# Kernel optimization log

Measured on AMD Instinct MI355X. Metric: run time of the kernel, lower is better.

Reference implementation:

```python
import jax, jax.numpy as jnp
import numpy as np

B, T, N, F, C, H, O = 4, 8, 4096, 32, 32, 64, 1
RADIUS = 50.0   # adjacency_threshold on pairwise distance
EPS = 1e-5      # batchnorm eps


def setup_inputs() -> dict:
    key = jax.random.key(0)
    ks = jax.random.split(key, 8)
    x = jax.random.normal(ks[0], (B, T, N, F), jnp.float32)
    # dist_mat from random 2D node locations in a 1000x1000 area; avg degree ~32
    loc = jax.random.uniform(ks[1], (N, 2), jnp.float32) * 1000.0
    d2 = jnp.sum((loc[:, None, :] - loc[None, :, :]) ** 2, axis=-1)  # [N,N]
    adj = (d2 < RADIUS ** 2).astype(jnp.float32)                     # includes self (d=0)
    dinv = 1.0 / jnp.sqrt(jnp.maximum(adj.sum(-1), 1.0))
    adj_norm = adj * dinv[:, None] * dinv[None, :]                   # D^-1/2 A D^-1/2
    s = 0.05
    return dict(
        x=x,
        adj_norm=adj_norm,
        bn_gamma=jnp.ones((F,), jnp.float32),
        bn_beta=jnp.zeros((F,), jnp.float32),
        W_gcn=jax.random.normal(ks[2], (F, C), jnp.float32) * s,
        b_gcn=jnp.zeros((C,), jnp.float32),
        W_ih=jax.random.normal(ks[3], (C, 3 * H), jnp.float32) * s,
        W_hh=jax.random.normal(ks[4], (H, 3 * H), jnp.float32) * s,
        b_ih=jnp.zeros((3 * H,), jnp.float32),
        b_hh=jnp.zeros((3 * H,), jnp.float32),
        W_dense=jax.random.normal(ks[5], (H, O), jnp.float32) * s,
        b_dense=jnp.zeros((O,), jnp.float32),
    )


def reference(x, adj_norm, bn_gamma, bn_beta, W_gcn, b_gcn, W_ih, W_hh, b_ih, b_hh, W_dense, b_dense):
    # BatchNorm2d over feature channel (training-mode batch stats, biased var)
    mean = x.mean(axis=(0, 1, 2))
    var = x.var(axis=(0, 1, 2))
    xn = (x - mean) * jax.lax.rsqrt(var + EPS) * bn_gamma + bn_beta  # [B,T,N,F]
    # GCN association (same math every timestep -> batch over T)
    ya = jnp.einsum('mn,btnf->btmf', adj_norm, xn)                   # neighbor aggregate
    y = jnp.einsum('btnf,fc->btnc', ya, W_gcn) + b_gcn               # [B,T,N,C]
    # precompute input-gate projections, then scan GRU cell over time
    gi = jnp.einsum('btnc,ch->btnh', y, W_ih) + b_ih                 # [B,T,N,3H]
    gi = jnp.transpose(gi, (1, 0, 2, 3))                             # [T,B,N,3H]

    def step(h, g):
        gh = h @ W_hh + b_hh
        r = jax.nn.sigmoid(g[..., :H] + gh[..., :H])
        z = jax.nn.sigmoid(g[..., H:2 * H] + gh[..., H:2 * H])
        n = jnp.tanh(g[..., 2 * H:] + r * gh[..., 2 * H:])
        h_new = (1.0 - z) * n + z * h
        return h_new, h_new

    h0 = jnp.zeros((B, N, H), x.dtype)
    _, hs = jax.lax.scan(step, h0, gi)                               # [T,B,N,H]
    out = jnp.transpose(hs, (1, 0, 2, 3)) @ W_dense + b_dense        # [B,T,N,O]
    return out
```

## Files before the change

kernel.cpp:

```cpp
#include <hip/hip_runtime.h>
#include <hip/hip_bf16.h>
#include <stdint.h>

#define B_ 4
#define T_ 8
#define N_ 4096
#define F_ 32
#define BT_ (B_*T_)
#define ROWS_ (B_*N_)
#define CAP_ 128
#define EPS_ 1e-5f
#define NELEM_ (B_*T_*N_*F_)

#define WS_BNP    0
#define WS_ROWSUM 16384
#define WS_DEG    (WS_ROWSUM + 4096)
#define WS_FRG    (WS_DEG + 4096)
#define WS_PAIR   (WS_FRG + 52*256)
#define WS_XA     (WS_PAIR + 4096*CAP_*2)
#define WS_X16    (WS_XA + NELEM_)

typedef float v4f __attribute__((ext_vector_type(4)));
typedef _Float16 half8 __attribute__((ext_vector_type(8)));
union HU { uint32_t u[4]; half8 v; };

__device__ inline float sigm_f(float x) {
  return __builtin_amdgcn_rcpf(1.0f + __expf(-x));
}
__device__ inline uint32_t f16pair(float a, float b) {
  union { _Float16 h; unsigned short s; } x, y;
  x.h = (_Float16)a; y.h = (_Float16)b;
  return (uint32_t)x.s | ((uint32_t)y.s << 16);
}
__device__ inline void sp2(float a0, float a1, uint32_t& hi, uint32_t& lo) {
  _Float16 h0 = (_Float16)a0, h1 = (_Float16)a1;
  float r0 = a0 - (float)h0, r1 = a1 - (float)h1;
  union { _Float16 h; unsigned short s; } u0, u1, v0, v1;
  u0.h = h0; u1.h = h1; v0.h = (_Float16)r0; v1.h = (_Float16)r1;
  hi = (uint32_t)u0.s | ((uint32_t)u1.s << 16);
  lo = (uint32_t)v0.s | ((uint32_t)v1.s << 16);
}

__global__ void __launch_bounds__(256)
k_pre(const float* __restrict__ x, const float* __restrict__ A, float* __restrict__ ws) {
  if (blockIdx.x < 2048) {
    int m0 = blockIdx.x * 2;
    __shared__ int cnt[2];
    __shared__ float wsum[4][2];
    if (threadIdx.x < 2) cnt[threadIdx.x] = 0;
    __syncthreads();
    int* deg = (int*)&ws[WS_DEG];
    float2* pair = (float2*)&ws[WS_PAIR];
    const float4* A4 = (const float4*)(A + (size_t)m0 * N_);
    float4 av4[8];
#pragma unroll
    for (int r = 0; r < 2; r++)
#pragma unroll
      for (int i = 0; i < 4; i++) av4[r * 4 + i] = A4[r * 1024 + threadIdx.x + 256 * i];
    float lsum[2] = {0.f, 0.f};
#pragma unroll
    for (int r = 0; r < 2; r++)
#pragma unroll
      for (int i = 0; i < 4; i++) {
        float av[4] = {av4[r*4+i].x, av4[r*4+i].y, av4[r*4+i].z, av4[r*4+i].w};
        int nb4 = (threadIdx.x + 256 * i) * 4;
#pragma unroll
        for (int e = 0; e < 4; e++) {
          float a = av[e];
          if (a != 0.0f) {
            int p = atomicAdd(&cnt[r], 1);
            if (p < CAP_) pair[(size_t)(m0 + r) * CAP_ + p] = make_float2(__int_as_float((nb4 + e) * F_), a);
            lsum[r] += a;
          }
        }
      }
#pragma unroll
    for (int r = 0; r < 2; r++) {
      float s = lsum[r];
#pragma unroll
      for (int off = 32; off > 0; off >>= 1) s += __shfl_xor(s, off, 64);
      if ((threadIdx.x & 63) == 0) wsum[threadIdx.x >> 6][r] = s;
    }
    __syncthreads();
#pragma unroll
    for (int r = 0; r < 2; r++) {
      int c = cnt[r];
      for (int p = c + threadIdx.x; p < 68; p += 256)
        pair[(size_t)(m0 + r) * CAP_ + p] = make_float2(__int_as_float(0), 0.0f);
    }
    if (threadIdx.x < 2) {
      int r = threadIdx.x;
      deg[m0 + r] = min(cnt[r], CAP_);
      ws[WS_ROWSUM + m0 + r] = wsum[0][r] + wsum[1][r] + wsum[2][r] + wsum[3][r];
    }
  } else {
    int bnb = blockIdx.x - 2048;
    const float4* x4 = (const float4*)x;
    uint2* x16 = (uint2*)(ws + WS_X16);
    int tid = bnb * 256 + threadIdx.x;
    float s[4] = {0,0,0,0}, s2[4] = {0,0,0,0};
    for (int i = tid; i < NELEM_ / 4; i += 256 * 256) {
      float4 v = x4[i];
      s[0] += v.x; s2[0] += v.x * v.x;
      s[1] += v.y; s2[1] += v.y * v.y;
      s[2] += v.z; s2[2] += v.z * v.z;
      s[3] += v.w; s2[3] += v.w * v.w;
      int bt = i >> 15, rem = i & 32767, n = rem >> 3, f4 = rem & 7;
      uint2 hp;
      hp.x = f16pair(v.x, v.y);
      hp.y = f16pair(v.z, v.w);
      x16[(size_t)(n * 32 + bt) * 8 + f4] = hp;
    }
    __shared__ float ls[256][4], ls2[256][4];
#pragma unroll
    for (int r = 0; r < 4; r++) { ls[threadIdx.x][r] = s[r]; ls2[threadIdx.x][r] = s2[r]; }
    __syncthreads();
    int t = threadIdx.x;
    if (t < 32) {
      int g = t >> 2, r = t & 3;
      float a = 0.f;
      for (int q = g; q < 256; q += 8) a += ls[q][r];
      ws[WS_BNP + bnb * 64 + t] = a;
    } else if (t < 64) {
      int cch = t - 32;
      int g = cch >> 2, r = cch & 3;
      float b2 = 0.f;
      for (int q = g; q < 256; q += 8) b2 += ls2[q][r];
      ws[WS_BNP + bnb * 64 + t] = b2;
    }
  }
}

#define AGG_STEP(d) { \
    float vv = pv[d]; \
    half8 t0 = pb0[d], t1 = pb1[d]; \
    float2 p = pl[wid * 69 + k + 4 + d]; \
    int nb = __float_as_int(p.x) << 5; \
    pv[d] = p.y; \
    pb0[d] = *(const half8*)(xT + nb + lo0); \
    pb1[d] = *(const half8*)(xT + nb + lo1); \
    _Pragma("unroll") \
    for (int j = 0; j < 8; j++) { \
      acc0[j] += vv * (float)t0[j]; \
      acc1[j] += vv * (float)t1[j]; } }

__global__ void __launch_bounds__(256, 4)
k_aggf(const float* __restrict__ x, const float* __restrict__ gamma,
       const float* __restrict__ beta, const float* __restrict__ Wg,
       const float* __restrict__ bg, const float* __restrict__ Wih,
       const float* __restrict__ bih, const float* __restrict__ Whh,
       const float* __restrict__ bhh, float* __restrict__ ws) {
  __shared__ float2 pl[32 * 69];
  int tid = threadIdx.x;
  if (blockIdx.x >= 1024) {
    float* fs   = (float*)pl;
    float* bnp4 = fs;
    float* bns  = fs + 256;
    float* scl  = fs + 320;
    float* shf  = fs + 352;
    float* ps   = fs + 384;
    float* Wg_s = fs + 416;
    float* Wic  = fs + 1440;
    float* Wxc  = fs + 1952;
    float* UsV  = fs + 2464;
    float* Whc  = fs + 2496;
    int fi = blockIdx.x - 1024;
    int mt, kt;
    if (fi < 32)      { mt = fi >> 2;              kt = fi & 3; }
    else if (fi < 40) { mt = 8 + ((fi - 32) >> 1); kt = (fi & 1) ? 3 : 0; }
    else              { int r = fi - 40; mt = 12 + r / 3; kt = 1 + r % 3; }
    int cls = mt >> 2;
    int colbase = (cls < 2) ? mt * 16 : 128 + (mt & 3) * 16;
    if (kt == 1 || kt == 2) {
      for (int e = tid; e < 512; e += 256) {
        int r = e >> 4, cc = e & 15;
        Whc[e] = Whh[(size_t)((kt - 1) * 32 + r) * 192 + colbase + cc];
      }
    } else {
      ((float4*)Wg_s)[tid] = ((const float4*)Wg)[tid];
      for (int e = tid; e < 512; e += 256) {
        int r = e >> 4, cc = e & 15;
        Wic[e] = Wih[(size_t)r * 192 + colbase + cc];
      }
      int g = tid >> 6, cch = tid & 63;
      float a = 0.f;
      for (int i = 0; i < 64; i++) a += ws[WS_BNP + (size_t)(g + 4 * i) * 64 + cch];
      bnp4[g * 64 + cch] = a;
    }
    __syncthreads();
    if ((kt == 0 || kt == 3) && tid < 64)
      bns[tid] = bnp4[tid] + bnp4[64 + tid] + bnp4[128 + tid] + bnp4[192 + tid];
    __syncthreads();
    if ((kt == 0 || kt == 3) && tid < 32) {
      float cntf = (float)(B_ * T_ * N_);
      float mean = bns[tid] / cntf;
      float var = bns[32 + tid] / cntf - mean * mean;
      float sc = gamma[tid] * rsqrtf(var + EPS_);
      scl[tid] = sc;
      shf[tid] = beta[tid] - mean * sc;
    }
    __syncthreads();
    if (kt == 3 && tid < 32) {
      float acc = 0.f;
#pragma unroll
      for (int f = 0; f < 32; f++) acc += shf[f] * Wg_s[f * 32 + tid];
      ps[tid] = acc;
    }
    __syncthreads();
    if (kt == 0) {
      for (int e = tid; e < 512; e += 256) {
        int f = e >> 4, cc = e & 15;
        float acc = 0.f;
#pragma unroll
        for (int m = 0; m < 32; m++) acc += Wg_s[f * 32 + m] * Wic[m * 16 + cc];
        Wxc[e] = scl[f] * acc;
      }
    } else if (kt == 3) {
      if (tid < 16) {
        float au = 0.f;
#pragma unroll
        for (int c2 = 0; c2 < 32; c2++) au += ps[c2] * Wic[c2 * 16 + tid];
        UsV[tid] = au;
      } else if (tid < 32) {
        int cc = tid - 16;
        float av = 0.f;
#pragma unroll
        for (int c2 = 0; c2 < 32; c2++) av += bg[c2] * Wic[c2 * 16 + cc];
        UsV[16 + cc] = av + bih[colbase + cc];
      }
    }
    __syncthreads();
    if (tid < 64) {
      int L = tid, q = L >> 4, c = L & 15;
      uint32_t* wsu = (uint32_t*)ws;
#pragma unroll
      for (int d = 0; d < 4; d++) {
        float a01[2];
#pragma unroll
        for (int h2 = 0; h2 < 2; h2++) {
          int kk = q * 8 + 2 * d + h2;
          float v;
          if (kt == 0)       v = Wxc[kk * 16 + c];
          else if (kt != 3)  v = Whc[kk * 16 + c];
          else if (kk == 0)  v = (cls == 3) ? 0.f : UsV[c];
          else if (kk == 1)  v = (cls < 2) ? (UsV[16 + c] + bhh[colbase + c])
                                           : (cls == 2 ? UsV[16 + c] : bhh[colbase + c]);
          else               v = 0.f;
          a01[h2] = v;
        }
        wsu[WS_FRG + fi * 256 + L * 4 + d] = f16pair(a01[0], a01[1]);
      }
    }
    return;
  }
  int m0 = blockIdx.x * 4;
  int wid = tid >> 6, L = tid & 63;
  int m = m0 + wid;
  const int* deg = (const int*)&ws[WS_DEG];
  const float2* pair = (const float2*)&ws[WS_PAIR];
  for (int qq = tid; qq < 4 * 68; qq += 256) {
    int r = qq / 68, sl = qq - r * 68;
    pl[r * 69 + sl] = pair[(size_t)(m0 + r) * CAP_ + sl];
  }
  __syncthreads();
  int d0 = deg[m];
  int dm = min(d0, 64);
  int bound = (dm + 3) & ~3;
  const _Float16* xT = (const _Float16*)(ws + WS_X16);
  int lo0 = L * 8, lo1 = 512 + L * 8;
  float acc0[8], acc1[8];
#pragma unroll
  for (int j = 0; j < 8; j++) { acc0[j] = 0.f; acc1[j] = 0.f; }
  half8 pb0[4], pb1[4];
  float pv[4];
#pragma unroll
  for (int d = 0; d < 4; d++) {
    float2 p = pl[wid * 69 + d];
    int nb = __float_as_int(p.x) << 5;
    pv[d] = p.y;
    pb0[d] = *(const half8*)(xT + nb + lo0);
    pb1[d] = *(const half8*)(xT + nb + lo1);
  }
  for (int k = 0; k < bound; k += 4) {
    AGG_STEP(0) AGG_STEP(1) AGG_STEP(2) AGG_STEP(3)
  }
  if (d0 > 64) {
    for (int k = 64; k < d0; k++) {
      float2 p = pair[(size_t)m * CAP_ + k];
      int nb = __float_as_int(p.x) << 5;
      float vv = p.y;
      half8 t0 = *(const half8*)(xT + nb + lo0);
      half8 t1 = *(const half8*)(xT + nb + lo1);
#pragma unroll
      for (int j = 0; j < 8; j++) {
        acc0[j] += vv * (float)t0[j];
        acc1[j] += vv * (float)t1[j];
      }
    }
  }
  int s0 = L >> 2, cg = (L & 3) * 8;
  size_t ob0 = ((size_t)s0 * N_ + m) * F_ + cg;
  size_t ob1 = ((size_t)(s0 + 16) * N_ + m) * F_ + cg;
  v4f w0a = {acc0[0], acc0[1], acc0[2], acc0[3]};
  v4f w0b = {acc0[4], acc0[5], acc0[6], acc0[7]};
  v4f w1a = {acc1[0], acc1[1], acc1[2], acc1[3]};
  v4f w1b = {acc1[4], acc1[5], acc1[6], acc1[7]};
  *(v4f*)(ws + WS_XA + ob0) = w0a;
  *(v4f*)(ws + WS_XA + ob0 + 4) = w0b;
  *(v4f*)(ws + WS_XA + ob1) = w1a;
  *(v4f*)(ws + WS_XA + ob1 + 4) = w1b;
}

#define LDA(fi) (*(const half8*)(frg + (fi)*256 + L*4))
#define DO1(A_, fi, BH, BL) { half8 af = LDA(fi); \
  A_ = __builtin_amdgcn_mfma_f32_16x16x32_f16(af, BH, A_, 0, 0, 0); \
  A_ = __builtin_amdgcn_mfma_f32_16x16x32_f16(af, BL, A_, 0, 0, 0); }
#define DO1C(A_, C_, fi, BH, BL) { half8 af = LDA(fi); \
  A_ = __builtin_amdgcn_mfma_f32_16x16x32_f16(af, BH, C_, 0, 0, 0); \
  A_ = __builtin_amdgcn_mfma_f32_16x16x32_f16(af, BL, A_, 0, 0, 0); }
#define LBAR() { asm volatile("s_waitcnt lgkmcnt(0)" ::: "memory"); \
  __builtin_amdgcn_s_barrier(); \
  __builtin_amdgcn_sched_barrier(0); }

__global__ void __launch_bounds__(256, 2)
k_gru(const float* __restrict__ Wd, const float* __restrict__ bd,
      const float* __restrict__ ws, float* __restrict__ out) {
  __shared__ uint32_t frg[52 * 256];
  __shared__ uint32_t hx[2][2][1344];
  __shared__ float obuf[2][8][16];
  {
    const uint4* gf = (const uint4*)(ws + WS_FRG);
    uint4* sf = (uint4*)frg;
    for (int i = threadIdx.x; i < 52 * 64; i += 256) sf[i] = gf[i];
  }
  __syncthreads();
  int wid = threadIdx.x >> 6, L = threadIdx.x & 63;
  int grp = wid >> 1, half = wid & 1, h2 = half * 2;
  int q = L >> 4, c = L & 15;
  int rg0 = blockIdx.x * 32 + grp * 16;
  int b = rg0 >> 12;
  int node0 = rg0 & (N_ - 1);
  int fR0 = 4 * h2, fR1 = 4 * h2 + 4;
  int fZ0 = 16 + 4 * h2, fZ1 = 20 + 4 * h2;
  int fN0 = 32 + 2 * h2, fN1 = 34 + 2 * h2;
  int fG0 = 40 + 3 * h2, fG1 = 43 + 3 * h2;
  float wdv[2][4];
#pragma unroll
  for (int lg = 0; lg < 2; lg++)
#pragma unroll
    for (int r = 0; r < 4; r++) wdv[lg][r] = Wd[16 * (h2 + lg) + 4 * q + r];
  float bdv = bd[0];

  const float* xab = ws + WS_XA;
  float4 xaA[T_], xaB[T_];
#pragma unroll
  for (int t = 0; t < T_; t++) {
    size_t xo = ((size_t)(b * T_ + t) * N_ + node0 + c) * F_ + q * 8;
    xaA[t] = *(const float4*)(xab + xo);
    xaB[t] = *(const float4*)(xab + xo + 4);
  }

  HU b3h, b3l;
#pragma unroll
  for (int d = 0; d < 4; d++) { b3h.u[d] = 0; b3l.u[d] = 0; }
  {
    float rsv = ws[WS_ROWSUM + node0 + c];
    uint32_t rhi, rlo;
    sp2(rsv, 1.0f, rhi, rlo);
    if (q == 0) { b3h.u[0] = rhi; b3l.u[0] = rlo & 0xFFFFu; }
  }

  v4f bias[8];
  {
    v4f z4 = {0.f, 0.f, 0.f, 0.f};
    DO1C(bias[0], z4, fR0 + 3, b3h.v, b3l.v)
    DO1C(bias[1], z4, fR1 + 3, b3h.v, b3l.v)
    DO1C(bias[2], z4, fZ0 + 3, b3h.v, b3l.v)
    DO1C(bias[3], z4, fZ1 + 3, b3h.v, b3l.v)
    DO1C(bias[4], z4, fN0 + 1, b3h.v, b3l.v)
    DO1C(bias[5], z4, fN1 + 1, b3h.v, b3l.v)
    DO1C(bias[6], z4, fG0 + 2, b3h.v, b3l.v)
    DO1C(bias[7], z4, fG1 + 2, b3h.v, b3l.v)
  }

  float h[2][4];
#pragma unroll
  for (int lg = 0; lg < 2; lg++)
#pragma unroll
    for (int r = 0; r < 4; r++) h[lg][r] = 0.f;
  float o8[T_];

#pragma unroll
  for (int t = 0; t < T_; t++) {
    HU b1h, b1l, b2h, b2l;
    if (t > 0) {
      const uint32_t* hb = hx[grp][(t - 1) & 1];
#pragma unroll
      for (int d = 0; d < 4; d++) {
        b1h.u[d] = hb[((4 * q + d) * 2 + 0) * 21 + c];
        b1l.u[d] = hb[((4 * q + d) * 2 + 1) * 21 + c];
        b2h.u[d] = hb[((16 + 4 * q + d) * 2 + 0) * 21 + c];
        b2l.u[d] = hb[((16 + 4 * q + d) * 2 + 1) * 21 + c];
      }
    }
    HU b0h, b0l;
    sp2(xaA[t].x, xaA[t].y, b0h.u[0], b0l.u[0]);
    sp2(xaA[t].z, xaA[t].w, b0h.u[1], b0l.u[1]);
    sp2(xaB[t].x, xaB[t].y, b0h.u[2], b0l.u[2]);
    sp2(xaB[t].z, xaB[t].w, b0h.u[3], b0l.u[3]);
    v4f acc[8];
    if (t > 0) {
      DO1C(acc[0], bias[0], fR0 + 1, b1h.v, b1l.v)
      DO1C(acc[1], bias[1], fR1 + 1, b1h.v, b1l.v)
      DO1C(acc[2], bias[2], fZ0 + 1, b1h.v, b1l.v)
      DO1C(acc[3], bias[3], fZ1 + 1, b1h.v, b1l.v)
      DO1C(acc[6], bias[6], fG0,     b1h.v, b1l.v)
      DO1C(acc[7], bias[7], fG1,     b1h.v, b1l.v)
      DO1(acc[0], fR0 + 2, b2h.v, b2l.v)
      DO1(acc[1], fR1 + 2, b2h.v, b2l.v)
      DO1(acc[2], fZ0 + 2, b2h.v, b2l.v)
      DO1(acc[3], fZ1 + 2, b2h.v, b2l.v)
      DO1(acc[6], fG0 + 1, b2h.v, b2l.v)
      DO1(acc[7], fG1 + 1, b2h.v, b2l.v)
      DO1(acc[0], fR0, b0h.v, b0l.v)
      DO1(acc[1], fR1, b0h.v, b0l.v)
      DO1(acc[2], fZ0, b0h.v, b0l.v)
      DO1(acc[3], fZ1, b0h.v, b0l.v)
      DO1C(acc[4], bias[4], fN0, b0h.v, b0l.v)
      DO1C(acc[5], bias[5], fN1, b0h.v, b0l.v)
    } else {
      DO1C(acc[0], bias[0], fR0, b0h.v, b0l.v)
      DO1C(acc[1], bias[1], fR1, b0h.v, b0l.v)
      DO1C(acc[2], bias[2], fZ0, b0h.v, b0l.v)
      DO1C(acc[3], bias[3], fZ1, b0h.v, b0l.v)
      DO1C(acc[4], bias[4], fN0, b0h.v, b0l.v)
      DO1C(acc[5], bias[5], fN1, b0h.v, b0l.v)
      acc[6] = bias[6]; acc[7] = bias[7];
    }
    float o = 0.f;
#pragma unroll
    for (int lg = 0; lg < 2; lg++)
#pragma unroll
      for (int r = 0; r < 4; r++) {
        float rr = sigm_f(acc[lg][r]);
        float zz = sigm_f(acc[2 + lg][r]);
        float nn = 2.0f * sigm_f(2.0f * (acc[4 + lg][r] + rr * acc[6 + lg][r])) - 1.0f;
        float hn = zz * (h[lg][r] - nn) + nn;
        h[lg][r] = hn;
        o += wdv[lg][r] * hn;
      }
    o += __shfl_xor(o, 16, 64);
    o += __shfl_xor(o, 32, 64);
    o8[t] = o;
    if (t < T_ - 1) {
      uint32_t* hb = hx[grp][t & 1];
#pragma unroll
      for (int lg = 0; lg < 2; lg++)
#pragma unroll
        for (int rp = 0; rp < 2; rp++) {
          uint32_t phi, plo;
          sp2(h[lg][2 * rp], h[lg][2 * rp + 1], phi, plo);
          int pidx = 8 * (h2 + lg) + 2 * q + rp;
          hb[(pidx * 2 + 0) * 21 + c] = phi;
          hb[(pidx * 2 + 1) * 21 + c] = plo;
        }
      LBAR()
    }
  }
  if (half == 1 && L < 16) {
#pragma unroll
    for (int t = 0; t < T_; t++) obuf[grp][t][L] = o8[t];
  }
  LBAR()
  if (half == 0 && L < 16) {
#pragma unroll
    for (int t = 0; t < T_; t++)
      out[(size_t)(b * T_ + t) * N_ + node0 + L] = o8[t] + obuf[grp][t][L] + bdv;
  }
}

extern "C" void kernel_launch(void* const* d_in, const int* in_sizes, int n_in,
                              void* d_out, int out_size, void* d_ws, size_t ws_size,
                              hipStream_t stream) {
  const float* x     = (const float*)d_in[0];
  const float* adj   = (const float*)d_in[1];
  const float* gamma = (const float*)d_in[2];
  const float* beta  = (const float*)d_in[3];
  const float* Wg    = (const float*)d_in[4];
  const float* bg    = (const float*)d_in[5];
  const float* Wih   = (const float*)d_in[6];
  const float* Whh   = (const float*)d_in[7];
  const float* bih   = (const float*)d_in[8];
  const float* bhh   = (const float*)d_in[9];
  const float* Wd    = (const float*)d_in[10];
  const float* bd    = (const float*)d_in[11];
  float* ws = (float*)d_ws;
  float* out = (float*)d_out;

  k_pre<<<2048 + 256, 256, 0, stream>>>(x, adj, ws);
  k_aggf<<<1024 + 52, 256, 0, stream>>>(x, gamma, beta, Wg, bg, Wih, bih, Whh, bhh, ws);
  k_gru<<<512, 256, 0, stream>>>(Wd, bd, ws, out);
}
```

Before: 168.2 us.

## Fuse three kernels into one persistent kernel with grid barriers

Merges the preprocessing, aggregation/fragment-building and GRU kernels into a single persistent launch of 512 blocks. The phases are separated by atomic-counter grid barriers, and the counters are reset by a memset before each launch. This removes kernel launch gaps and inter-kernel drain, but the fused kernel runs the early phases at the GRU kernel's occupancy (launch_bounds 256,2 with large shared memory) and with only 512 blocks looping over the work. It also relies on all 512 blocks being co-resident, or the spin barrier deadlocks.

```diff
diff --git a/kernel.cpp b/kernel.cpp
--- a/kernel.cpp
+++ b/kernel.cpp
@@ -19,6 +19,7 @@
 #define WS_PAIR   (WS_FRG + 52*256)
 #define WS_XA     (WS_PAIR + 4096*CAP_*2)
 #define WS_X16    (WS_XA + NELEM_)
+#define WS_BAR    8000000
 
 typedef float v4f __attribute__((ext_vector_type(4)));
 typedef _Float16 half8 __attribute__((ext_vector_type(8)));
@@ -41,94 +42,15 @@
   lo = (uint32_t)v0.s | ((uint32_t)v1.s << 16);
 }
 
-__global__ void __launch_bounds__(256)
-k_pre(const float* __restrict__ x, const float* __restrict__ A, float* __restrict__ ws) {
-  if (blockIdx.x < 2048) {
-    int m0 = blockIdx.x * 2;
-    __shared__ int cnt[2];
-    __shared__ float wsum[4][2];
-    if (threadIdx.x < 2) cnt[threadIdx.x] = 0;
-    __syncthreads();
-    int* deg = (int*)&ws[WS_DEG];
-    float2* pair = (float2*)&ws[WS_PAIR];
-    const float4* A4 = (const float4*)(A + (size_t)m0 * N_);
-    float4 av4[8];
-#pragma unroll
-    for (int r = 0; r < 2; r++)
-#pragma unroll
-      for (int i = 0; i < 4; i++) av4[r * 4 + i] = A4[r * 1024 + threadIdx.x + 256 * i];
-    float lsum[2] = {0.f, 0.f};
-#pragma unroll
-    for (int r = 0; r < 2; r++)
-#pragma unroll
-      for (int i = 0; i < 4; i++) {
-        float av[4] = {av4[r*4+i].x, av4[r*4+i].y, av4[r*4+i].z, av4[r*4+i].w};
-        int nb4 = (threadIdx.x + 256 * i) * 4;
-#pragma unroll
-        for (int e = 0; e < 4; e++) {
-          float a = av[e];
-          if (a != 0.0f) {
-            int p = atomicAdd(&cnt[r], 1);
-            if (p < CAP_) pair[(size_t)(m0 + r) * CAP_ + p] = make_float2(__int_as_float((nb4 + e) * F_), a);
-            lsum[r] += a;
-          }
-        }
-      }
-#pragma unroll
-    for (int r = 0; r < 2; r++) {
-      float s = lsum[r];
-#pragma unroll
-      for (int off = 32; off > 0; off >>= 1) s += __shfl_xor(s, off, 64);
-      if ((threadIdx.x & 63) == 0) wsum[threadIdx.x >> 6][r] = s;
-    }
-    __syncthreads();
-#pragma unroll
-    for (int r = 0; r < 2; r++) {
-      int c = cnt[r];
-      for (int p = c + threadIdx.x; p < 68; p += 256)
-        pair[(size_t)(m0 + r) * CAP_ + p] = make_float2(__int_as_float(0), 0.0f);
-    }
-    if (threadIdx.x < 2) {
-      int r = threadIdx.x;
-      deg[m0 + r] = min(cnt[r], CAP_);
-      ws[WS_ROWSUM + m0 + r] = wsum[0][r] + wsum[1][r] + wsum[2][r] + wsum[3][r];
-    }
-  } else {
-    int bnb = blockIdx.x - 2048;
-    const float4* x4 = (const float4*)x;
-    uint2* x16 = (uint2*)(ws + WS_X16);
-    int tid = bnb * 256 + threadIdx.x;
-    float s[4] = {0,0,0,0}, s2[4] = {0,0,0,0};
-    for (int i = tid; i < NELEM_ / 4; i += 256 * 256) {
-      float4 v = x4[i];
-      s[0] += v.x; s2[0] += v.x * v.x;
-      s[1] += v.y; s2[1] += v.y * v.y;
-      s[2] += v.z; s2[2] += v.z * v.z;
-      s[3] += v.w; s2[3] += v.w * v.w;
-      int bt = i >> 15, rem = i & 32767, n = rem >> 3, f4 = rem & 7;
-      uint2 hp;
-      hp.x = f16pair(v.x, v.y);
-      hp.y = f16pair(v.z, v.w);
-      x16[(size_t)(n * 32 + bt) * 8 + f4] = hp;
-    }
-    __shared__ float ls[256][4], ls2[256][4];
-#pragma unroll
-    for (int r = 0; r < 4; r++) { ls[threadIdx.x][r] = s[r]; ls2[threadIdx.x][r] = s2[r]; }
-    __syncthreads();
-    int t = threadIdx.x;
-    if (t < 32) {
-      int g = t >> 2, r = t & 3;
-      float a = 0.f;
-      for (int q = g; q < 256; q += 8) a += ls[q][r];
-      ws[WS_BNP + bnb * 64 + t] = a;
-    } else if (t < 64) {
-      int cch = t - 32;
-      int g = cch >> 2, r = cch & 3;
-      float b2 = 0.f;
-      for (int q = g; q < 256; q += 8) b2 += ls2[q][r];
-      ws[WS_BNP + bnb * 64 + t] = b2;
-    }
+__device__ inline void grid_bar(int* c) {
+  __syncthreads();
+  if (threadIdx.x == 0) {
+    __threadfence();
+    atomicAdd(c, 1);
+    while (atomicAdd(c, 0) < 512) __builtin_amdgcn_s_sleep(4);
+    __threadfence();
   }
+  __syncthreads();
 }
 
 #define AGG_STEP(d) { \
@@ -144,173 +66,6 @@
       acc0[j] += vv * (float)t0[j]; \
       acc1[j] += vv * (float)t1[j]; } }
 
-__global__ void __launch_bounds__(256, 4)
-k_aggf(const float* __restrict__ x, const float* __restrict__ gamma,
-       const float* __restrict__ beta, const float* __restrict__ Wg,
-       const float* __restrict__ bg, const float* __restrict__ Wih,
-       const float* __restrict__ bih, const float* __restrict__ Whh,
-       const float* __restrict__ bhh, float* __restrict__ ws) {
-  __shared__ float2 pl[32 * 69];
-  int tid = threadIdx.x;
-  if (blockIdx.x >= 1024) {
-    float* fs   = (float*)pl;
-    float* bnp4 = fs;
-    float* bns  = fs + 256;
-    float* scl  = fs + 320;
-    float* shf  = fs + 352;
-    float* ps   = fs + 384;
-    float* Wg_s = fs + 416;
-    float* Wic  = fs + 1440;
-    float* Wxc  = fs + 1952;
-    float* UsV  = fs + 2464;
-    float* Whc  = fs + 2496;
-    int fi = blockIdx.x - 1024;
-    int mt, kt;
-    if (fi < 32)      { mt = fi >> 2;              kt = fi & 3; }
-    else if (fi < 40) { mt = 8 + ((fi - 32) >> 1); kt = (fi & 1) ? 3 : 0; }
-    else              { int r = fi - 40; mt = 12 + r / 3; kt = 1 + r % 3; }
-    int cls = mt >> 2;
-    int colbase = (cls < 2) ? mt * 16 : 128 + (mt & 3) * 16;
-    if (kt == 1 || kt == 2) {
-      for (int e = tid; e < 512; e += 256) {
-        int r = e >> 4, cc = e & 15;
-        Whc[e] = Whh[(size_t)((kt - 1) * 32 + r) * 192 + colbase + cc];
-      }
-    } else {
-      ((float4*)Wg_s)[tid] = ((const float4*)Wg)[tid];
-      for (int e = tid; e < 512; e += 256) {
-        int r = e >> 4, cc = e & 15;
-        Wic[e] = Wih[(size_t)r * 192 + colbase + cc];
-      }
-      int g = tid >> 6, cch = tid & 63;
-      float a = 0.f;
-      for (int i = 0; i < 64; i++) a += ws[WS_BNP + (size_t)(g + 4 * i) * 64 + cch];
-      bnp4[g * 64 + cch] = a;
-    }
-    __syncthreads();
-    if ((kt == 0 || kt == 3) && tid < 64)
-      bns[tid] = bnp4[tid] + bnp4[64 + tid] + bnp4[128 + tid] + bnp4[192 + tid];
-    __syncthreads();
-    if ((kt == 0 || kt == 3) && tid < 32) {
-      float cntf = (float)(B_ * T_ * N_);
-      float mean = bns[tid] / cntf;
-      float var = bns[32 + tid] / cntf - mean * mean;
-      float sc = gamma[tid] * rsqrtf(var + EPS_);
-      scl[tid] = sc;
-      shf[tid] = beta[tid] - mean * sc;
-    }
-    __syncthreads();
-    if (kt == 3 && tid < 32) {
-      float acc = 0.f;
-#pragma unroll
-      for (int f = 0; f < 32; f++) acc += shf[f] * Wg_s[f * 32 + tid];
-      ps[tid] = acc;
-    }
-    __syncthreads();
-    if (kt == 0) {
-      for (int e = tid; e < 512; e += 256) {
-        int f = e >> 4, cc = e & 15;
-        float acc = 0.f;
-#pragma unroll
-        for (int m = 0; m < 32; m++) acc += Wg_s[f * 32 + m] * Wic[m * 16 + cc];
-        Wxc[e] = scl[f] * acc;
-      }
-    } else if (kt == 3) {
-      if (tid < 16) {
-        float au = 0.f;
-#pragma unroll
-        for (int c2 = 0; c2 < 32; c2++) au += ps[c2] * Wic[c2 * 16 + tid];
-        UsV[tid] = au;
-      } else if (tid < 32) {
-        int cc = tid - 16;
-        float av = 0.f;
-#pragma unroll
-        for (int c2 = 0; c2 < 32; c2++) av += bg[c2] * Wic[c2 * 16 + cc];
-        UsV[16 + cc] = av + bih[colbase + cc];
-      }
-    }
-    __syncthreads();
-    if (tid < 64) {
-      int L = tid, q = L >> 4, c = L & 15;
-      uint32_t* wsu = (uint32_t*)ws;
-#pragma unroll
-      for (int d = 0; d < 4; d++) {
-        float a01[2];
-#pragma unroll
-        for (int h2 = 0; h2 < 2; h2++) {
-          int kk = q * 8 + 2 * d + h2;
-          float v;
-          if (kt == 0)       v = Wxc[kk * 16 + c];
-          else if (kt != 3)  v = Whc[kk * 16 + c];
-          else if (kk == 0)  v = (cls == 3) ? 0.f : UsV[c];
-          else if (kk == 1)  v = (cls < 2) ? (UsV[16 + c] + bhh[colbase + c])
-                                           : (cls == 2 ? UsV[16 + c] : bhh[colbase + c]);
-          else               v = 0.f;
-          a01[h2] = v;
-        }
-        wsu[WS_FRG + fi * 256 + L * 4 + d] = f16pair(a01[0], a01[1]);
-      }
-    }
-    return;
-  }
-  int m0 = blockIdx.x * 4;
-  int wid = tid >> 6, L = tid & 63;
-  int m = m0 + wid;
-  const int* deg = (const int*)&ws[WS_DEG];
-  const float2* pair = (const float2*)&ws[WS_PAIR];
-  for (int qq = tid; qq < 4 * 68; qq += 256) {
-    int r = qq / 68, sl = qq - r * 68;
-    pl[r * 69 + sl] = pair[(size_t)(m0 + r) * CAP_ + sl];
-  }
-  __syncthreads();
-  int d0 = deg[m];
-  int dm = min(d0, 64);
-  int bound = (dm + 3) & ~3;
-  const _Float16* xT = (const _Float16*)(ws + WS_X16);
-  int lo0 = L * 8, lo1 = 512 + L * 8;
-  float acc0[8], acc1[8];
-#pragma unroll
-  for (int j = 0; j < 8; j++) { acc0[j] = 0.f; acc1[j] = 0.f; }
-  half8 pb0[4], pb1[4];
-  float pv[4];
-#pragma unroll
-  for (int d = 0; d < 4; d++) {
-    float2 p = pl[wid * 69 + d];
-    int nb = __float_as_int(p.x) << 5;
-    pv[d] = p.y;
-    pb0[d] = *(const half8*)(xT + nb + lo0);
-    pb1[d] = *(const half8*)(xT + nb + lo1);
-  }
-  for (int k = 0; k < bound; k += 4) {
-    AGG_STEP(0) AGG_STEP(1) AGG_STEP(2) AGG_STEP(3)
-  }
-  if (d0 > 64) {
-    for (int k = 64; k < d0; k++) {
-      float2 p = pair[(size_t)m * CAP_ + k];
-      int nb = __float_as_int(p.x) << 5;
-      float vv = p.y;
-      half8 t0 = *(const half8*)(xT + nb + lo0);
-      half8 t1 = *(const half8*)(xT + nb + lo1);
-#pragma unroll
-      for (int j = 0; j < 8; j++) {
-        acc0[j] += vv * (float)t0[j];
-        acc1[j] += vv * (float)t1[j];
-      }
-    }
-  }
-  int s0 = L >> 2, cg = (L & 3) * 8;
-  size_t ob0 = ((size_t)s0 * N_ + m) * F_ + cg;
-  size_t ob1 = ((size_t)(s0 + 16) * N_ + m) * F_ + cg;
-  v4f w0a = {acc0[0], acc0[1], acc0[2], acc0[3]};
-  v4f w0b = {acc0[4], acc0[5], acc0[6], acc0[7]};
-  v4f w1a = {acc1[0], acc1[1], acc1[2], acc1[3]};
-  v4f w1b = {acc1[4], acc1[5], acc1[6], acc1[7]};
-  *(v4f*)(ws + WS_XA + ob0) = w0a;
-  *(v4f*)(ws + WS_XA + ob0 + 4) = w0b;
-  *(v4f*)(ws + WS_XA + ob1) = w1a;
-  *(v4f*)(ws + WS_XA + ob1 + 4) = w1b;
-}
-
 #define LDA(fi) (*(const half8*)(frg + (fi)*256 + L*4))
 #define DO1(A_, fi, BH, BL) { half8 af = LDA(fi); \
   A_ = __builtin_amdgcn_mfma_f32_16x16x32_f16(af, BH, A_, 0, 0, 0); \
@@ -323,159 +78,426 @@
   __builtin_amdgcn_sched_barrier(0); }
 
 __global__ void __launch_bounds__(256, 2)
-k_gru(const float* __restrict__ Wd, const float* __restrict__ bd,
-      const float* __restrict__ ws, float* __restrict__ out) {
+k_all(const float* __restrict__ x, const float* __restrict__ A,
+      const float* __restrict__ gamma, const float* __restrict__ beta,
+      const float* __restrict__ Wg, const float* __restrict__ bg,
+      const float* __restrict__ Wih, const float* __restrict__ bih,
+      const float* __restrict__ Whh, const float* __restrict__ bhh,
+      const float* __restrict__ Wd, const float* __restrict__ bd,
+      float* __restrict__ ws, float* __restrict__ out) {
   __shared__ uint32_t frg[52 * 256];
   __shared__ uint32_t hx[2][2][1344];
   __shared__ float obuf[2][8][16];
+  int tid = threadIdx.x;
+  int* bar = (int*)(ws + WS_BAR);
+
+  for (int u = blockIdx.x; u < 2304; u += 512) {
+    if (u < 2048) {
+      int m0 = u * 2;
+      int* cnt = (int*)frg;
+      float* wsum = (float*)(frg + 2);
+      if (tid < 2) cnt[tid] = 0;
+      __syncthreads();
+      int* deg = (int*)&ws[WS_DEG];
+      float2* pair = (float2*)&ws[WS_PAIR];
+      const float4* A4 = (const float4*)(A + (size_t)m0 * N_);
+      float4 av4[8];
+#pragma unroll
+      for (int r = 0; r < 2; r++)
+#pragma unroll
+        for (int i = 0; i < 4; i++) av4[r * 4 + i] = A4[r * 1024 + tid + 256 * i];
+      float lsum[2] = {0.f, 0.f};
+#pragma unroll
+      for (int r = 0; r < 2; r++)
+#pragma unroll
+        for (int i = 0; i < 4; i++) {
+          float av[4] = {av4[r*4+i].x, av4[r*4+i].y, av4[r*4+i].z, av4[r*4+i].w};
+          int nb4 = (tid + 256 * i) * 4;
+#pragma unroll
+          for (int e = 0; e < 4; e++) {
+            float a = av[e];
+            if (a != 0.0f) {
+              int p = atomicAdd(&cnt[r], 1);
+              if (p < CAP_) pair[(size_t)(m0 + r) * CAP_ + p] = make_float2(__int_as_float((nb4 + e) * F_), a);
+              lsum[r] += a;
+            }
+          }
+        }
+#pragma unroll
+      for (int r = 0; r < 2; r++) {
+        float s = lsum[r];
+#pragma unroll
+        for (int off = 32; off > 0; off >>= 1) s += __shfl_xor(s, off, 64);
+        if ((tid & 63) == 0) wsum[(tid >> 6) * 2 + r] = s;
+      }
+      __syncthreads();
+#pragma unroll
+      for (int r = 0; r < 2; r++) {
+        int c = cnt[r];
+        for (int p = c + tid; p < 68; p += 256)
+          pair[(size_t)(m0 + r) * CAP_ + p] = make_float2(__int_as_float(0), 0.0f);
+      }
+      if (tid < 2) {
+        int r = tid;
+        deg[m0 + r] = min(cnt[r], CAP_);
+        ws[WS_ROWSUM + m0 + r] = wsum[0 * 2 + r] + wsum[1 * 2 + r] + wsum[2 * 2 + r] + wsum[3 * 2 + r];
+      }
+      __syncthreads();
+    } else {
+      int bnb = u - 2048;
+      const float4* x4 = (const float4*)x;
+      uint2* x16 = (uint2*)(ws + WS_X16);
+      int gt = bnb * 256 + tid;
+      float s[4] = {0,0,0,0}, s2[4] = {0,0,0,0};
+      for (int i = gt; i < NELEM_ / 4; i += 256 * 256) {
+        float4 v = x4[i];
+        s[0] += v.x; s2[0] += v.x * v.x;
+        s[1] += v.y; s2[1] += v.y * v.y;
+        s[2] += v.z; s2[2] += v.z * v.z;
+        s[3] += v.w; s2[3] += v.w * v.w;
+        int bt = i >> 15, rem = i & 32767, n = rem >> 3, f4 = rem & 7;
+        uint2 hp;
+        hp.x = f16pair(v.x, v.y);
+        hp.y = f16pair(v.z, v.w);
+        x16[(size_t)(n * 32 + bt) * 8 + f4] = hp;
+      }
+      float* ls  = (float*)frg;
+      float* ls2 = (float*)(frg + 1024);
+#pragma unroll
+      for (int r = 0; r < 4; r++) { ls[tid * 4 + r] = s[r]; ls2[tid * 4 + r] = s2[r]; }
+      __syncthreads();
+      int t = tid;
+      if (t < 32) {
+        int g = t >> 2, r = t & 3;
+        float a = 0.f;
+        for (int q = g; q < 256; q += 8) a += ls[q * 4 + r];
+        ws[WS_BNP + bnb * 64 + t] = a;
+      } else if (t < 64) {
+        int cch = t - 32;
+        int g = cch >> 2, r = cch & 3;
+        float b2 = 0.f;
+        for (int q = g; q < 256; q += 8) b2 += ls2[q * 4 + r];
+        ws[WS_BNP + bnb * 64 + t] = b2;
+      }
+      __syncthreads();
+    }
+  }
+  grid_bar(bar + 0);
+
+  for (int u = blockIdx.x; u < 1076; u += 512) {
+    if (u >= 1024) {
+      float* fs   = (float*)frg;
+      float* bnp4 = fs;
+      float* bns  = fs + 256;
+      float* scl  = fs + 320;
+      float* shf  = fs + 352;
+      float* ps   = fs + 384;
+      float* Wg_s = fs + 416;
+      float* Wic  = fs + 1440;
+      float* Wxc  = fs + 1952;
+      float* UsV  = fs + 2464;
+      float* Whc  = fs + 2496;
+      int fi = u - 1024;
+      int mt, kt;
+      if (fi < 32)      { mt = fi >> 2;              kt = fi & 3; }
+      else if (fi < 40) { mt = 8 + ((fi - 32) >> 1); kt = (fi & 1) ? 3 : 0; }
+      else              { int r = fi - 40; mt = 12 + r / 3; kt = 1 + r % 3; }
+      int cls = mt >> 2;
+      int colbase = (cls < 2) ? mt * 16 : 128 + (mt & 3) * 16;
+      if (kt == 1 || kt == 2) {
+        for (int e = tid; e < 512; e += 256) {
+          int r = e >> 4, cc = e & 15;
+          Whc[e] = Whh[(size_t)((kt - 1) * 32 + r) * 192 + colbase + cc];
+        }
+      } else {
+        ((float4*)Wg_s)[tid] = ((const float4*)Wg)[tid];
+        for (int e = tid; e < 512; e += 256) {
+          int r = e >> 4, cc = e & 15;
+          Wic[e] = Wih[(size_t)r * 192 + colbase + cc];
+        }
+        int g = tid >> 6, cch = tid & 63;
+        float a = 0.f;
+        for (int i = 0; i < 64; i++) a += ws[WS_BNP + (size_t)(g + 4 * i) * 64 + cch];
+        bnp4[g * 64 + cch] = a;
+      }
+      __syncthreads();
+      if ((kt == 0 || kt == 3) && tid < 64)
+        bns[tid] = bnp4[tid] + bnp4[64 + tid] + bnp4[128 + tid] + bnp4[192 + tid];
+      __syncthreads();
+      if ((kt == 0 || kt == 3) && tid < 32) {
+        float cntf = (float)(B_ * T_ * N_);
+        float mean = bns[tid] / cntf;
+        float var = bns[32 + tid] / cntf - mean * mean;
+        float sc = gamma[tid] * rsqrtf(var + EPS_);
+        scl[tid] = sc;
+        shf[tid] = beta[tid] - mean * sc;
+      }
+      __syncthreads();
+      if (kt == 3 && tid < 32) {
+        float acc = 0.f;
+#pragma unroll
+        for (int f = 0; f < 32; f++) acc += shf[f] * Wg_s[f * 32 + tid];
+        ps[tid] = acc;
+      }
+      __syncthreads();
+      if (kt == 0) {
+        for (int e = tid; e < 512; e += 256) {
+          int f = e >> 4, cc = e & 15;
+          float acc = 0.f;
+#pragma unroll
+          for (int m = 0; m < 32; m++) acc += Wg_s[f * 32 + m] * Wic[m * 16 + cc];
+          Wxc[e] = scl[f] * acc;
+        }
+      } else if (kt == 3) {
+        if (tid < 16) {
+          float au = 0.f;
+#pragma unroll
+          for (int c2 = 0; c2 < 32; c2++) au += ps[c2] * Wic[c2 * 16 + tid];
+          UsV[tid] = au;
+        } else if (tid < 32) {
+          int cc = tid - 16;
+          float av = 0.f;
+#pragma unroll
+          for (int c2 = 0; c2 < 32; c2++) av += bg[c2] * Wic[c2 * 16 + cc];
+          UsV[16 + cc] = av + bih[colbase + cc];
+        }
+      }
+      __syncthreads();
+      if (tid < 64) {
+        int L = tid, q = L >> 4, c = L & 15;
+        uint32_t* wsu = (uint32_t*)ws;
+#pragma unroll
+        for (int d = 0; d < 4; d++) {
+          float a01[2];
+#pragma unroll
+          for (int h2 = 0; h2 < 2; h2++) {
+            int kk = q * 8 + 2 * d + h2;
+            float v;
+            if (kt == 0)       v = Wxc[kk * 16 + c];
+            else if (kt != 3)  v = Whc[kk * 16 + c];
+            else if (kk == 0)  v = (cls == 3) ? 0.f : UsV[c];
+            else if (kk == 1)  v = (cls < 2) ? (UsV[16 + c] + bhh[colbase + c])
+                                             : (cls == 2 ? UsV[16 + c] : bhh[colbase + c]);
+            else               v = 0.f;
+            a01[h2] = v;
+          }
+          wsu[WS_FRG + fi * 256 + L * 4 + d] = f16pair(a01[0], a01[1]);
+        }
+      }
+      __syncthreads();
+    } else {
+      float2* pl = (float2*)frg;
+      int m0 = u * 4;
+      int wid = tid >> 6, L = tid & 63;
+      int m = m0 + wid;
+      const int* deg = (const int*)&ws[WS_DEG];
+      const float2* pair = (const float2*)&ws[WS_PAIR];
+      for (int qq = tid; qq < 4 * 68; qq += 256) {
+        int r = qq / 68, sl = qq - r * 68;
+        pl[r * 69 + sl] = pair[(size_t)(m0 + r) * CAP_ + sl];
+      }
+      __syncthreads();
+      int d0 = deg[m];
+      int dm = min(d0, 64);
+      int bound = (dm + 3) & ~3;
+      const _Float16* xT = (const _Float16*)(ws + WS_X16);
+      int lo0 = L * 8, lo1 = 512 + L * 8;
+      float acc0[8], acc1[8];
+#pragma unroll
+      for (int j = 0; j < 8; j++) { acc0[j] = 0.f; acc1[j] = 0.f; }
+      half8 pb0[4], pb1[4];
+      float pv[4];
+#pragma unroll
+      for (int d = 0; d < 4; d++) {
+        float2 p = pl[wid * 69 + d];
+        int nb = __float_as_int(p.x) << 5;
+        pv[d] = p.y;
+        pb0[d] = *(const half8*)(xT + nb + lo0);
+        pb1[d] = *(const half8*)(xT + nb + lo1);
+      }
+      for (int k = 0; k < bound; k += 4) {
+        AGG_STEP(0) AGG_STEP(1) AGG_STEP(2) AGG_STEP(3)
+      }
+      if (d0 > 64) {
+        for (int k = 64; k < d0; k++) {
+          float2 p = pair[(size_t)m * CAP_ + k];
+          int nb = __float_as_int(p.x) << 5;
+          float vv = p.y;
+          half8 t0 = *(const half8*)(xT + nb + lo0);
+          half8 t1 = *(const half8*)(xT + nb + lo1);
+#pragma unroll
+          for (int j = 0; j < 8; j++) {
+            acc0[j] += vv * (float)t0[j];
+            acc1[j] += vv * (float)t1[j];
+          }
+        }
+      }
+      int s0 = L >> 2, cg = (L & 3) * 8;
+      size_t ob0 = ((size_t)s0 * N_ + m) * F_ + cg;
+      size_t ob1 = ((size_t)(s0 + 16) * N_ + m) * F_ + cg;
+      v4f w0a = {acc0[0], acc0[1], acc0[2], acc0[3]};
+      v4f w0b = {acc0[4], acc0[5], acc0[6], acc0[7]};
+      v4f w1a = {acc1[0], acc1[1], acc1[2], acc1[3]};
+      v4f w1b = {acc1[4], acc1[5], acc1[6], acc1[7]};
+      *(v4f*)(ws + WS_XA + ob0) = w0a;
+      *(v4f*)(ws + WS_XA + ob0 + 4) = w0b;
+      *(v4f*)(ws + WS_XA + ob1) = w1a;
+      *(v4f*)(ws + WS_XA + ob1 + 4) = w1b;
+      __syncthreads();
+    }
+  }
+  grid_bar(bar + 1);
+
   {
-    const uint4* gf = (const uint4*)(ws + WS_FRG);
-    uint4* sf = (uint4*)frg;
-    for (int i = threadIdx.x; i < 52 * 64; i += 256) sf[i] = gf[i];
-  }
-  __syncthreads();
-  int wid = threadIdx.x >> 6, L = threadIdx.x & 63;
-  int grp = wid >> 1, half = wid & 1, h2 = half * 2;
-  int q = L >> 4, c = L & 15;
-  int rg0 = blockIdx.x * 32 + grp * 16;
-  int b = rg0 >> 12;
-  int node0 = rg0 & (N_ - 1);
-  int fR0 = 4 * h2, fR1 = 4 * h2 + 4;
-  int fZ0 = 16 + 4 * h2, fZ1 = 20 + 4 * h2;
-  int fN0 = 32 + 2 * h2, fN1 = 34 + 2 * h2;
-  int fG0 = 40 + 3 * h2, fG1 = 43 + 3 * h2;
-  float wdv[2][4];
-#pragma unroll
-  for (int lg = 0; lg < 2; lg++)
-#pragma unroll
-    for (int r = 0; r < 4; r++) wdv[lg][r] = Wd[16 * (h2 + lg) + 4 * q + r];
-  float bdv = bd[0];
-
-  const float* xab = ws + WS_XA;
-  float4 xaA[T_], xaB[T_];
-#pragma unroll
-  for (int t = 0; t < T_; t++) {
-    size_t xo = ((size_t)(b * T_ + t) * N_ + node0 + c) * F_ + q * 8;
-    xaA[t] = *(const float4*)(xab + xo);
-    xaB[t] = *(const float4*)(xab + xo + 4);
-  }
-
-  HU b3h, b3l;
-#pragma unroll
-  for (int d = 0; d < 4; d++) { b3h.u[d] = 0; b3l.u[d] = 0; }
-  {
-    float rsv = ws[WS_ROWSUM + node0 + c];
-    uint32_t rhi, rlo;
-    sp2(rsv, 1.0f, rhi, rlo);
-    if (q == 0) { b3h.u[0] = rhi; b3l.u[0] = rlo & 0xFFFFu; }
-  }
-
-  v4f bias[8];
-  {
-    v4f z4 = {0.f, 0.f, 0.f, 0.f};
-    DO1C(bias[0], z4, fR0 + 3, b3h.v, b3l.v)
-    DO1C(bias[1], z4, fR1 + 3, b3h.v, b3l.v)
-    DO1C(bias[2], z4, fZ0 + 3, b3h.v, b3l.v)
-    DO1C(bias[3], z4, fZ1 + 3, b3h.v, b3l.v)
-    DO1C(bias[4], z4, fN0 + 1, b3h.v, b3l.v)
-    DO1C(bias[5], z4, fN1 + 1, b3h.v, b3l.v)
-    DO1C(bias[6], z4, fG0 + 2, b3h.v, b3l.v)
-    DO1C(bias[7], z4, fG1 + 2, b3h.v, b3l.v)
-  }
-
-  float h[2][4];
-#pragma unroll
-  for (int lg = 0; lg < 2; lg++)
-#pragma unroll
-    for (int r = 0; r < 4; r++) h[lg][r] = 0.f;
-  float o8[T_];
-
-#pragma unroll
-  for (int t = 0; t < T_; t++) {
-    HU b1h, b1l, b2h, b2l;
-    if (t > 0) {
-      const uint32_t* hb = hx[grp][(t - 1) & 1];
-#pragma unroll
-      for (int d = 0; d < 4; d++) {
-        b1h.u[d] = hb[((4 * q + d) * 2 + 0) * 21 + c];
-        b1l.u[d] = hb[((4 * q + d) * 2 + 1) * 21 + c];
-        b2h.u[d] = hb[((16 + 4 * q + d) * 2 + 0) * 21 + c];
-        b2l.u[d] = hb[((16 + 4 * q + d) * 2 + 1) * 21 + c];
-      }
-    }
-    HU b0h, b0l;
-    sp2(xaA[t].x, xaA[t].y, b0h.u[0], b0l.u[0]);
-    sp2(xaA[t].z, xaA[t].w, b0h.u[1], b0l.u[1]);
-    sp2(xaB[t].x, xaB[t].y, b0h.u[2], b0l.u[2]);
-    sp2(xaB[t].z, xaB[t].w, b0h.u[3], b0l.u[3]);
-    v4f acc[8];
-    if (t > 0) {
-      DO1C(acc[0], bias[0], fR0 + 1, b1h.v, b1l.v)
-      DO1C(acc[1], bias[1], fR1 + 1, b1h.v, b1l.v)
-      DO1C(acc[2], bias[2], fZ0 + 1, b1h.v, b1l.v)
-      DO1C(acc[3], bias[3], fZ1 + 1, b1h.v, b1l.v)
-      DO1C(acc[6], bias[6], fG0,     b1h.v, b1l.v)
-      DO1C(acc[7], bias[7], fG1,     b1h.v, b1l.v)
-      DO1(acc[0], fR0 + 2, b2h.v, b2l.v)
-      DO1(acc[1], fR1 + 2, b2h.v, b2l.v)
-      DO1(acc[2], fZ0 + 2, b2h.v, b2l.v)
-      DO1(acc[3], fZ1 + 2, b2h.v, b2l.v)
-      DO1(acc[6], fG0 + 1, b2h.v, b2l.v)
-      DO1(acc[7], fG1 + 1, b2h.v, b2l.v)
-      DO1(acc[0], fR0, b0h.v, b0l.v)
-      DO1(acc[1], fR1, b0h.v, b0l.v)
-      DO1(acc[2], fZ0, b0h.v, b0l.v)
-      DO1(acc[3], fZ1, b0h.v, b0l.v)
-      DO1C(acc[4], bias[4], fN0, b0h.v, b0l.v)
-      DO1C(acc[5], bias[5], fN1, b0h.v, b0l.v)
-    } else {
-      DO1C(acc[0], bias[0], fR0, b0h.v, b0l.v)
-      DO1C(acc[1], bias[1], fR1, b0h.v, b0l.v)
-      DO1C(acc[2], bias[2], fZ0, b0h.v, b0l.v)
-      DO1C(acc[3], bias[3], fZ1, b0h.v, b0l.v)
-      DO1C(acc[4], bias[4], fN0, b0h.v, b0l.v)
-      DO1C(acc[5], bias[5], fN1, b0h.v, b0l.v)
-      acc[6] = bias[6]; acc[7] = bias[7];
-    }
-    float o = 0.f;
+    {
+      const uint4* gf = (const uint4*)(ws + WS_FRG);
+      uint4* sf = (uint4*)frg;
+      for (int i = tid; i < 52 * 64; i += 256) sf[i] = gf[i];
+    }
+    __syncthreads();
+    int wid = tid >> 6, L = tid & 63;
+    int grp = wid >> 1, half = wid & 1, h2 = half * 2;
+    int q = L >> 4, c = L & 15;
+    int rg0 = blockIdx.x * 32 + grp * 16;
+    int b = rg0 >> 12;
+    int node0 = rg0 & (N_ - 1);
+    int fR0 = 4 * h2, fR1 = 4 * h2 + 4;
+    int fZ0 = 16 + 4 * h2, fZ1 = 20 + 4 * h2;
+    int fN0 = 32 + 2 * h2, fN1 = 34 + 2 * h2;
+    int fG0 = 40 + 3 * h2, fG1 = 43 + 3 * h2;
+    float wdv[2][4];
 #pragma unroll
     for (int lg = 0; lg < 2; lg++)
 #pragma unroll
-      for (int r = 0; r < 4; r++) {
-        float rr = sigm_f(acc[lg][r]);
-        float zz = sigm_f(acc[2 + lg][r]);
-        float nn = 2.0f * sigm_f(2.0f * (acc[4 + lg][r] + rr * acc[6 + lg][r])) - 1.0f;
-        float hn = zz * (h[lg][r] - nn) + nn;
-        h[lg][r] = hn;
-        o += wdv[lg][r] * hn;
-      }
-    o += __shfl_xor(o, 16, 64);
-    o += __shfl_xor(o, 32, 64);
-    o8[t] = o;
-    if (t < T_ - 1) {
-      uint32_t* hb = hx[grp][t & 1];
+      for (int r = 0; r < 4; r++) wdv[lg][r] = Wd[16 * (h2 + lg) + 4 * q + r];
+    float bdv = bd[0];
+
+    const float* xab = ws + WS_XA;
+    float4 xaA[T_], xaB[T_];
+#pragma unroll
+    for (int t = 0; t < T_; t++) {
+      size_t xo = ((size_t)(b * T_ + t) * N_ + node0 + c) * F_ + q * 8;
+      xaA[t] = *(const float4*)(xab + xo);
+      xaB[t] = *(const float4*)(xab + xo + 4);
+    }
+
+    HU b3h, b3l;
+#pragma unroll
+    for (int d = 0; d < 4; d++) { b3h.u[d] = 0; b3l.u[d] = 0; }
+    {
+      float rsv = ws[WS_ROWSUM + node0 + c];
+      uint32_t rhi, rlo;
+      sp2(rsv, 1.0f, rhi, rlo);
+      if (q == 0) { b3h.u[0] = rhi; b3l.u[0] = rlo & 0xFFFFu; }
+    }
+
+    v4f bias[8];
+    {
+      v4f z4 = {0.f, 0.f, 0.f, 0.f};
+      DO1C(bias[0], z4, fR0 + 3, b3h.v, b3l.v)
+      DO1C(bias[1], z4, fR1 + 3, b3h.v, b3l.v)
+      DO1C(bias[2], z4, fZ0 + 3, b3h.v, b3l.v)
+      DO1C(bias[3], z4, fZ1 + 3, b3h.v, b3l.v)
+      DO1C(bias[4], z4, fN0 + 1, b3h.v, b3l.v)
+      DO1C(bias[5], z4, fN1 + 1, b3h.v, b3l.v)
+      DO1C(bias[6], z4, fG0 + 2, b3h.v, b3l.v)
+      DO1C(bias[7], z4, fG1 + 2, b3h.v, b3l.v)
+    }
+
+    float h[2][4];
+#pragma unroll
+    for (int lg = 0; lg < 2; lg++)
+#pragma unroll
+      for (int r = 0; r < 4; r++) h[lg][r] = 0.f;
+    float o8[T_];
+
+#pragma unroll
+    for (int t = 0; t < T_; t++) {
+      HU b1h, b1l, b2h, b2l;
+      if (t > 0) {
+        const uint32_t* hb = hx[grp][(t - 1) & 1];
+#pragma unroll
+        for (int d = 0; d < 4; d++) {
+          b1h.u[d] = hb[((4 * q + d) * 2 + 0) * 21 + c];
+          b1l.u[d] = hb[((4 * q + d) * 2 + 1) * 21 + c];
+          b2h.u[d] = hb[((16 + 4 * q + d) * 2 + 0) * 21 + c];
+          b2l.u[d] = hb[((16 + 4 * q + d) * 2 + 1) * 21 + c];
+        }
+      }
+      HU b0h, b0l;
+      sp2(xaA[t].x, xaA[t].y, b0h.u[0], b0l.u[0]);
+      sp2(xaA[t].z, xaA[t].w, b0h.u[1], b0l.u[1]);
+      sp2(xaB[t].x, xaB[t].y, b0h.u[2], b0l.u[2]);
+      sp2(xaB[t].z, xaB[t].w, b0h.u[3], b0l.u[3]);
+      v4f acc[8];
+      if (t > 0) {
+        DO1C(acc[0], bias[0], fR0 + 1, b1h.v, b1l.v)
+        DO1C(acc[1], bias[1], fR1 + 1, b1h.v, b1l.v)
+        DO1C(acc[2], bias[2], fZ0 + 1, b1h.v, b1l.v)
+        DO1C(acc[3], bias[3], fZ1 + 1, b1h.v, b1l.v)
+        DO1C(acc[6], bias[6], fG0,     b1h.v, b1l.v)
+        DO1C(acc[7], bias[7], fG1,     b1h.v, b1l.v)
+        DO1(acc[0], fR0 + 2, b2h.v, b2l.v)
+        DO1(acc[1], fR1 + 2, b2h.v, b2l.v)
+        DO1(acc[2], fZ0 + 2, b2h.v, b2l.v)
+        DO1(acc[3], fZ1 + 2, b2h.v, b2l.v)
+        DO1(acc[6], fG0 + 1, b2h.v, b2l.v)
+        DO1(acc[7], fG1 + 1, b2h.v, b2l.v)
+        DO1(acc[0], fR0, b0h.v, b0l.v)
+        DO1(acc[1], fR1, b0h.v, b0l.v)
+        DO1(acc[2], fZ0, b0h.v, b0l.v)
+        DO1(acc[3], fZ1, b0h.v, b0l.v)
+        DO1C(acc[4], bias[4], fN0, b0h.v, b0l.v)
+        DO1C(acc[5], bias[5], fN1, b0h.v, b0l.v)
+      } else {
+        DO1C(acc[0], bias[0], fR0, b0h.v, b0l.v)
+        DO1C(acc[1], bias[1], fR1, b0h.v, b0l.v)
+        DO1C(acc[2], bias[2], fZ0, b0h.v, b0l.v)
+        DO1C(acc[3], bias[3], fZ1, b0h.v, b0l.v)
+        DO1C(acc[4], bias[4], fN0, b0h.v, b0l.v)
+        DO1C(acc[5], bias[5], fN1, b0h.v, b0l.v)
+        acc[6] = bias[6]; acc[7] = bias[7];
+      }
+      float o = 0.f;
 #pragma unroll
       for (int lg = 0; lg < 2; lg++)
 #pragma unroll
-        for (int rp = 0; rp < 2; rp++) {
-          uint32_t phi, plo;
-          sp2(h[lg][2 * rp], h[lg][2 * rp + 1], phi, plo);
-          int pidx = 8 * (h2 + lg) + 2 * q + rp;
-          hb[(pidx * 2 + 0) * 21 + c] = phi;
-          hb[(pidx * 2 + 1) * 21 + c] = plo;
-        }
-      LBAR()
-    }
-  }
-  if (half == 1 && L < 16) {
-#pragma unroll
-    for (int t = 0; t < T_; t++) obuf[grp][t][L] = o8[t];
-  }
-  LBAR()
-  if (half == 0 && L < 16) {
-#pragma unroll
-    for (int t = 0; t < T_; t++)
-      out[(size_t)(b * T_ + t) * N_ + node0 + L] = o8[t] + obuf[grp][t][L] + bdv;
+        for (int r = 0; r < 4; r++) {
+          float rr = sigm_f(acc[lg][r]);
+          float zz = sigm_f(acc[2 + lg][r]);
+          float nn = 2.0f * sigm_f(2.0f * (acc[4 + lg][r] + rr * acc[6 + lg][r])) - 1.0f;
+          float hn = zz * (h[lg][r] - nn) + nn;
+          h[lg][r] = hn;
+          o += wdv[lg][r] * hn;
+        }
+      o += __shfl_xor(o, 16, 64);
+      o += __shfl_xor(o, 32, 64);
+      o8[t] = o;
+      if (t < T_ - 1) {
+        uint32_t* hb = hx[grp][t & 1];
+#pragma unroll
+        for (int lg = 0; lg < 2; lg++)
+#pragma unroll
+          for (int rp = 0; rp < 2; rp++) {
+            uint32_t phi, plo;
+            sp2(h[lg][2 * rp], h[lg][2 * rp + 1], phi, plo);
+            int pidx = 8 * (h2 + lg) + 2 * q + rp;
+            hb[(pidx * 2 + 0) * 21 + c] = phi;
+            hb[(pidx * 2 + 1) * 21 + c] = plo;
+          }
+        LBAR()
+      }
+    }
+    if (half == 1 && L < 16) {
+#pragma unroll
+      for (int t = 0; t < T_; t++) obuf[grp][t][L] = o8[t];
+    }
+    LBAR()
+    if (half == 0 && L < 16) {
+#pragma unroll
+      for (int t = 0; t < T_; t++)
+        out[(size_t)(b * T_ + t) * N_ + node0 + L] = o8[t] + obuf[grp][t][L] + bdv;
+    }
   }
 }
 
@@ -497,7 +519,7 @@
   float* ws = (float*)d_ws;
   float* out = (float*)d_out;
 
-  k_pre<<<2048 + 256, 256, 0, stream>>>(x, adj, ws);
-  k_aggf<<<1024 + 52, 256, 0, stream>>>(x, gamma, beta, Wg, bg, Wih, bih, Whh, bhh, ws);
-  k_gru<<<512, 256, 0, stream>>>(Wd, bd, ws, out);
+  hipMemsetAsync((char*)d_ws + (size_t)WS_BAR * 4, 0, 16, stream);
+  k_all<<<512, 256, 0, stream>>>(x, adj, gamma, beta, Wg, bg, Wih, bih,
+                                 Whh, bhh, Wd, bd, ws, out);
 }
```

Measured after the change: 286.3 us. +70.2%, slower.
